# Kernel optimization log

Hardware: AMD Instinct MI355X
Metric: run time of the kernel (lower is better)

## Reference

```python
import jax, jax.numpy as jnp
import numpy as np
from jax import lax

NUM_CLASSES = 16
IMAGE_SHAPE = (512, 512)
CONF_T = 0.05          # confidence_threshold (also NMS score_threshold)
IOU_T = 0.5            # nms_iou_threshold
MAX_PER_CLASS = 100    # max_detections_per_class
MAX_DET = 100          # max_detections
SIGMA = 0.05           # soft_nms_sigma
NEG = -1e10            # finite 'removed' score (always < CONF_T)


def _make_anchors(image_shape=IMAGE_SHAPE):
    # EfficientDet-style anchors: levels 3-7, anchor_scale=4, 3 scales x 3 ratios.
    # Format [cx, cy, w, h] in absolute pixels.
    H, W = image_shape
    out = []
    for level in range(3, 8):
        stride = 2 ** level
        base = float(stride) * 4.0
        fh, fw = H // stride, W // stride
        cx = (np.arange(fw) + 0.5) * stride
        cy = (np.arange(fh) + 0.5) * stride
        cxg, cyg = np.meshgrid(cx, cy)
        centers = np.stack([cxg, cyg], -1).reshape(-1, 1, 2)
        wh = np.array([[base * s * np.sqrt(r), base * s / np.sqrt(r)]
                       for s in (1.0, 2 ** (1.0 / 3.0), 2 ** (2.0 / 3.0))
                       for r in (0.5, 1.0, 2.0)])  # [9,2]
        a = np.concatenate([np.broadcast_to(centers, (fh * fw, 9, 2)),
                            np.broadcast_to(wh[None], (fh * fw, 9, 2))], -1)
        out.append(a.reshape(-1, 4))
    return np.concatenate(out, 0).astype(np.float32)  # [49104, 4]


def setup_inputs() -> dict:
    key = jax.random.key(0)
    N = 49104
    predictions = jax.random.normal(key, (4, N, 4 + NUM_CLASSES), dtype=jnp.float32)
    anchors = jnp.asarray(_make_anchors())
    return {"predictions": predictions, "anchors": anchors}


def _decode_boxes(box_pred, anchors):
    # box_variance is None -> no scaling. anchors [N,4] in [cx,cy,w,h].
    a = anchors[None]                                  # [1,N,4]
    xy = box_pred[..., :2] * a[..., 2:] + a[..., :2]   # centers
    wh = jnp.exp(box_pred[..., 2:]) * a[..., 2:]       # sizes
    return jnp.concatenate([xy - 0.5 * wh, xy + 0.5 * wh], -1)  # corners


def _pairwise_iou(sel, boxes):
    # sel [B,C,4], boxes [B,N,4] -> iou [B,C,N]
    lt = jnp.maximum(sel[:, :, None, :2], boxes[:, None, :, :2])
    rb = jnp.minimum(sel[:, :, None, 2:], boxes[:, None, :, 2:])
    wh = jnp.maximum(rb - lt, 0.0)
    inter = wh[..., 0] * wh[..., 1]
    area_s = (sel[..., 2] - sel[..., 0]) * (sel[..., 3] - sel[..., 1])
    area_b = (boxes[..., 2] - boxes[..., 0]) * (boxes[..., 3] - boxes[..., 1])
    union = area_s[:, :, None] + area_b[:, None, :] - inter
    return jnp.where(union > 0, inter / jnp.where(union > 0, union, 1.0), 0.0)


def _soft_nms(boxes, scores_init, remat=False):
    # Vectorized soft-NMS over all (batch, class) lanes simultaneously.
    # Matches tf.image.non_max_suppression_with_scores (Gaussian soft-NMS):
    # iteratively select max decayed score; hard-suppress iou>thr; decay
    # others by exp(-0.5/sigma * iou^2); stop when max < score_threshold.
    B, C, N = scores_init.shape
    scale = -0.5 / SIGMA
    n_idx = jnp.arange(N)

    def step(scores, _):
        idx = jnp.argmax(scores, axis=-1)                                   # [B,C]
        s = jnp.take_along_axis(scores, idx[..., None], axis=-1)[..., 0]    # [B,C]
        pick = s >= CONF_T
        sel = jax.vmap(lambda bx, ii: bx[ii])(boxes, idx)                   # [B,C,4]
        iou = _pairwise_iou(sel, boxes)                                     # [B,C,N]
        w = jnp.exp(scale * iou * iou)
        new = jnp.where(iou > IOU_T, NEG, scores * w)
        new = jnp.where(n_idx[None, None, :] == idx[..., None], NEG, new)
        scores = jnp.where(pick[..., None], new, scores)
        return scores, (idx, s, pick)

    if remat:
        step = jax.checkpoint(step)
    _, (idxs, sels, picks) = lax.scan(step, scores_init, None, length=MAX_PER_CLASS)
    tr = lambda x: jnp.moveaxis(x, 0, -1)  # [T,B,C] -> [B,C,T]
    return tr(idxs), tr(sels), tr(picks)


def _postprocess(boxes, idxs, sels, picks):
    # Per-class padding to MAX_PER_CLASS, class-major concat, compaction of
    # valid entries, then pad (<= MAX_DET) or stable top-MAX_DET by score.
    B, C, T = picks.shape
    M = C * T
    sel_boxes = jax.vmap(lambda bx, ii: bx[ii])(boxes, idxs.reshape(B, M))  # [B,M,4]
    scores_f = jnp.where(picks, sels, 0.0).reshape(B, M)
    boxes_f = jnp.where(picks.reshape(B, M, 1), sel_boxes, 0.0)
    cls_f = jnp.where(picks, jnp.arange(C, dtype=jnp.int32)[None, :, None],
                      jnp.int32(-1)).reshape(B, M)
    valid = picks.reshape(B, M)
    num_valid = jnp.sum(valid, axis=-1).astype(jnp.int32)                   # [B]

    # stable compaction: valid entries first, original (class-major) order kept
    order = jnp.argsort(jnp.logical_not(valid), axis=-1, stable=True)
    scf = jnp.take_along_axis(scores_f, order, -1)
    bxf = jnp.take_along_axis(boxes_f, order[..., None], 1)
    clf = jnp.take_along_axis(cls_f, order, -1)
    iv = jnp.arange(M)[None] < num_valid[:, None]
    scf = jnp.where(iv, scf, 0.0)
    bxf = jnp.where(iv[..., None], bxf, 0.0)
    clf = jnp.where(iv, clf, jnp.int32(-1))

    # overflow branch: stable descending sort by score over valid entries
    ordB = jnp.argsort(jnp.where(iv, -scf, jnp.inf), axis=-1, stable=True)[:, :MAX_DET]
    over = (num_valid > MAX_DET)[:, None]
    out_sc = jnp.where(over, jnp.take_along_axis(scf, ordB, -1), scf[:, :MAX_DET])
    out_bx = jnp.where(over[..., None],
                       jnp.take_along_axis(bxf, ordB[..., None], 1), bxf[:, :MAX_DET])
    out_cl = jnp.where(over, jnp.take_along_axis(clf, ordB, -1), clf[:, :MAX_DET])
    valid_det = jnp.minimum(num_valid, MAX_DET)
    return valid_det, out_bx, out_sc, out_cl


@jax.jit
def _forward(predictions, anchors):
    boxes = _decode_boxes(predictions[..., :4], anchors)          # [B,N,4]
    cls_prob = jax.nn.sigmoid(predictions[..., 4:])               # [B,N,C]
    max_cls = jnp.argmax(cls_prob, -1)                            # [B,N]
    max_score = jnp.max(cls_prob, -1)
    keep = max_score >= CONF_T
    C = cls_prob.shape[-1]
    cls_mask = (max_cls[:, None, :] == jnp.arange(C)[None, :, None]) & keep[:, None, :]
    scores_init = jnp.where(cls_mask, jnp.swapaxes(cls_prob, 1, 2), NEG)   # [B,C,N]
    idxs, sels, picks = _soft_nms(boxes, scores_init)
    return _postprocess(boxes, idxs, sels, picks)


def reference(predictions, anchors):
    # returns (valid_detections [B], nmsed_boxes [B,100,4],
    #          nmsed_scores [B,100], nmsed_classes [B,100])
    return _forward(predictions, anchors)
```

## Files before the change

kernel.cpp:

```cpp
#include <hip/hip_runtime.h>
#include <math.h>

#define CONF_T 0.05f
#define NEGF  -1e10f
#define NCLS 16
#define TDET 100
#define CAP 4096
#define MSEL 512
#define MTOT (NCLS*TDET)

template<int CTRL>
__device__ __forceinline__ void dpp_comb(float& s, int& j) {
  int si_ = __builtin_amdgcn_update_dpp(__float_as_int(s), __float_as_int(s),
                                        CTRL, 0xf, 0xf, false);
  int ji_ = __builtin_amdgcn_update_dpp(j, j, CTRL, 0xf, 0xf, false);
  float si = __int_as_float(si_);
  bool take = (si > s) || (si == s && ji_ < j);
  s = take ? si : s;
  j = take ? ji_ : j;
}
template<int CTRL>
__device__ __forceinline__ void dpp_max1(float& s) {
  int si_ = __builtin_amdgcn_update_dpp(__float_as_int(s), __float_as_int(s),
                                        CTRL, 0xf, 0xf, false);
  s = fmaxf(s, __int_as_float(si_));
}
template<int CTRL, int RM, bool BC>
__device__ __forceinline__ int dpp_mov0(int v) {
  return __builtin_amdgcn_update_dpp(0, v, CTRL, RM, 0xf, BC);
}
#define ROW_SHR1  0x111
#define ROW_SHR2  0x112
#define ROW_SHR4  0x114
#define ROW_SHR8  0x118
#define ROW_BC15  0x142
#define ROW_BC31  0x143

__device__ __forceinline__ void wave_comb64(float& s, int& j) {
  dpp_comb<ROW_SHR1>(s, j);
  dpp_comb<ROW_SHR2>(s, j);
  dpp_comb<ROW_SHR4>(s, j);
  dpp_comb<ROW_SHR8>(s, j);
  dpp_comb<ROW_BC15>(s, j);
  dpp_comb<ROW_BC31>(s, j);
}
__device__ __forceinline__ void wave_fmax64(float& s) {
  dpp_max1<ROW_SHR1>(s);
  dpp_max1<ROW_SHR2>(s);
  dpp_max1<ROW_SHR4>(s);
  dpp_max1<ROW_SHR8>(s);
  dpp_max1<ROW_BC15>(s);
  dpp_max1<ROW_BC31>(s);
}
__device__ __forceinline__ float rl_f(float v, int l) {
  return __int_as_float(__builtin_amdgcn_readlane(__float_as_int(v), l));
}

__global__ __launch_bounds__(256) void k_decode(
    const float* __restrict__ pred, const float* __restrict__ anch,
    float* __restrict__ boxes, float* __restrict__ score, int* __restrict__ cls,
    int* __restrict__ counts, int N, int nchunk)
{
  #pragma clang fp contract(off)
  const int b = blockIdx.x / nchunk;
  const int chunk = blockIdx.x % nchunk;
  const int t = threadIdx.x;
  const int n = chunk * 256 + t;

  __shared__ int hist[NCLS];
  if (t < NCLS) hist[t] = 0;
  __syncthreads();

  int v = -1;
  if (n < N) {
    const size_t i = (size_t)b * N + n;
    const float4* p4 = reinterpret_cast<const float4*>(pred + i * 20);
    float4 v0 = p4[0], v1 = p4[1], v2 = p4[2], v3 = p4[3], v4 = p4[4];
    float4 a = reinterpret_cast<const float4*>(anch)[n];
    float xx = v0.x * a.z + a.x;
    float yy = v0.y * a.w + a.y;
    float wx = expf(v0.z) * a.z;
    float wy = expf(v0.w) * a.w;
    float hx = 0.5f * wx, hy = 0.5f * wy;
    float4 bx;
    bx.x = xx - hx; bx.y = yy - hy; bx.z = xx + hx; bx.w = yy + hy;
    reinterpret_cast<float4*>(boxes)[i] = bx;

    float lg[NCLS] = {v1.x, v1.y, v1.z, v1.w, v2.x, v2.y, v2.z, v2.w,
                      v3.x, v3.y, v3.z, v3.w, v4.x, v4.y, v4.z, v4.w};
    float best = -1.0f; int bi = 0;
    #pragma unroll
    for (int c = 0; c < NCLS; ++c) {
      float s = 1.0f / (1.0f + expf(-lg[c]));
      if (s > best) { best = s; bi = c; }
    }
    score[i] = best;
    v = (best >= CONF_T) ? bi : -1;
    cls[i] = v;
  }

  int lane = t & 63;
  #pragma unroll
  for (int c = 0; c < NCLS; ++c) {
    unsigned long long bl = __ballot(v == c);
    if (lane == 0 && bl) atomicAdd(&hist[c], __popcll(bl));
  }
  __syncthreads();
  if (t < NCLS) counts[(b * NCLS + t) * nchunk + chunk] = hist[t];
}

__global__ __launch_bounds__(256) void k_scatter(
    const float* __restrict__ score, const int* __restrict__ cls,
    const float* __restrict__ boxes, const int* __restrict__ counts,
    float* __restrict__ cand_sc, float* __restrict__ cand_bx, int* __restrict__ ktot,
    int N, int nchunk)
{
  const int b = blockIdx.x / nchunk;
  const int chunk = blockIdx.x % nchunk;
  const int t = threadIdx.x;
  const int n = chunk * 256 + t;

  __shared__ int s_part[NCLS][17];
  __shared__ int s_ptot[NCLS][17];
  __shared__ int s_off[NCLS];
  __shared__ int wcnt[4][NCLS];

  {
    int c = t >> 4, part = t & 15;
    int su = 0, tot = 0;
    for (int ch = part; ch < nchunk; ch += 16) {
      int vv = counts[(b * NCLS + c) * nchunk + ch];
      tot += vv;
      su += (ch < chunk) ? vv : 0;
    }
    s_part[c][part] = su;
    s_ptot[c][part] = tot;
  }
  __syncthreads();
  if (t < NCLS) {
    int su = 0, tot = 0;
    #pragma unroll
    for (int i = 0; i < 16; ++i) { su += s_part[t][i]; tot += s_ptot[t][i]; }
    s_off[t] = su;
    if (chunk == 0) ktot[b * NCLS + t] = tot;
  }

  int v = (n < N) ? cls[(size_t)b * N + n] : -1;
  int lane = t & 63, w = t >> 6;
  int myrank = 0;
  #pragma unroll
  for (int c = 0; c < NCLS; ++c) {
    unsigned long long bl = __ballot(v == c);
    if (lane == 0) wcnt[w][c] = __popcll(bl);
    if (v == c) myrank = __popcll(bl & ((1ull << lane) - 1ull));
  }
  __syncthreads();
  if (v >= 0) {
    int pre = 0;
    #pragma unroll
    for (int i = 0; i < 4; ++i) if (i < w) pre += wcnt[i][v];
    int pos = s_off[v] + pre + myrank;
    if (pos < CAP) {
      int bc = b * NCLS + v;
      cand_sc[(size_t)bc * CAP + pos] = score[(size_t)b * N + n];
      reinterpret_cast<float4*>(cand_bx)[(size_t)bc * CAP + pos] =
          reinterpret_cast<const float4*>(boxes)[(size_t)b * N + n];
    }
  }
}

__global__ __launch_bounds__(512) void k_nms(
    const float* __restrict__ cand_sc, const float* __restrict__ cand_bx,
    const int* __restrict__ ktot,
    float* __restrict__ out_box, float* __restrict__ out_sc, int* __restrict__ out_pick,
    int* __restrict__ flagOK)
{
  #pragma clang fp contract(off)
  const int bc = blockIdx.x;
  const int t = threadIdx.x;
  const int lane = t & 63, w = t >> 6;

  __shared__ int    hist[4096];
  __shared__ int    s_wsum[8];
  __shared__ int    s_T, s_thrbits;
  __shared__ int    s_cc[8][8];
  __shared__ float  s_csc[MSEL];
  __shared__ float4 sbx[MSEL];
  __shared__ float4 pubA[2][8];
  __shared__ float2 pubB[2][8];
  __shared__ int    s_pk[TDET];
  __shared__ float  s_ps[TDET];

  int K = ktot[bc]; if (K > CAP) K = CAP;

  for (int i = t; i < 4096; i += 512) hist[i] = 0;
  if (t == 0) { s_T = 4096; s_thrbits = 0; }
  __syncthreads();

  float sc[8]; int key[8];
  #pragma unroll
  for (int k = 0; k < 8; ++k) {
    int j = k * 512 + t;
    if (j < K) {
      sc[k] = cand_sc[(size_t)bc * CAP + j];
      int bits = __float_as_int(sc[k]);
      int kk = (bits >> 11) - 0x7E000;
      kk = kk < 0 ? 0 : (kk > 4095 ? 4095 : kk);
      key[k] = kk;
      atomicAdd(&hist[kk], 1);
    } else { key[k] = -1; sc[k] = 0.0f; }
  }
  __syncthreads();

  int h[8]; int loc = 0;
  #pragma unroll
  for (int u = 0; u < 8; ++u) { h[u] = hist[8 * t + u]; loc += h[u]; }
  int pf = loc;
  pf += dpp_mov0<ROW_SHR1, 0xf, true >(pf);
  pf += dpp_mov0<ROW_SHR2, 0xf, true >(pf);
  pf += dpp_mov0<ROW_SHR4, 0xf, true >(pf);
  pf += dpp_mov0<ROW_SHR8, 0xf, true >(pf);
  pf += dpp_mov0<ROW_BC15, 0xa, false>(pf);
  pf += dpp_mov0<ROW_BC31, 0xc, false>(pf);
  if (lane == 63) s_wsum[w] = pf;
  __syncthreads();
  int base = 0, Kall = 0;
  #pragma unroll
  for (int i = 0; i < 8; ++i) {
    int v = s_wsum[i];
    Kall += v;
    if (i < w) base += v;
  }
  {
    int cLE = base + pf;
    int run = Kall - (cLE - loc);
    int cand = 0x7fffffff;
    #pragma unroll
    for (int u = 0; u < 8; ++u) {
      if (cand == 0x7fffffff && run <= MSEL) cand = 8 * t + u;
      run -= h[u];
    }
    if (cand != 0x7fffffff) atomicMin(&s_T, cand);
  }
  __syncthreads();
  const int T = s_T;

  unsigned long long bl0, bl1, bl2, bl3, bl4, bl5, bl6, bl7;
  #define KEEPP(k) ((key[k] >= 0) && (key[k] >= T))
  bl0 = __ballot(KEEPP(0)); bl1 = __ballot(KEEPP(1));
  bl2 = __ballot(KEEPP(2)); bl3 = __ballot(KEEPP(3));
  bl4 = __ballot(KEEPP(4)); bl5 = __ballot(KEEPP(5));
  bl6 = __ballot(KEEPP(6)); bl7 = __ballot(KEEPP(7));
  if (lane == 0) {
    s_cc[w][0] = __popcll(bl0); s_cc[w][1] = __popcll(bl1);
    s_cc[w][2] = __popcll(bl2); s_cc[w][3] = __popcll(bl3);
    s_cc[w][4] = __popcll(bl4); s_cc[w][5] = __popcll(bl5);
    s_cc[w][6] = __popcll(bl6); s_cc[w][7] = __popcll(bl7);
  }
  #pragma unroll
  for (int k = 0; k < 8; ++k)
    if (key[k] >= 0 && key[k] < T) atomicMax(&s_thrbits, __float_as_int(sc[k]));
  __syncthreads();

  int runpos = 0;
  #pragma unroll
  for (int k = 0; k < 8; ++k) {
    int pre = 0, tot = 0;
    #pragma unroll
    for (int i = 0; i < 8; ++i) {
      int c = s_cc[i][k];
      tot += c;
      if (i < w) pre += c;
    }
    unsigned long long blk = (k == 0) ? bl0 : (k == 1) ? bl1 : (k == 2) ? bl2 :
                             (k == 3) ? bl3 : (k == 4) ? bl4 : (k == 5) ? bl5 :
                             (k == 6) ? bl6 : bl7;
    if (KEEPP(k)) {
      int pos = runpos + pre + __popcll(blk & ((1ull << lane) - 1ull));
      s_csc[pos] = sc[k];
      sbx[pos] = reinterpret_cast<const float4*>(cand_bx)[(size_t)bc * CAP + k * 512 + t];
    }
    runpos += tot;
  }
  #undef KEEPP
  const int KM = runpos;
  const float thr = (T == 0) ? -1e30f : __int_as_float(s_thrbits);
  __syncthreads();

  float  rsc0; float4 rbx0; float rar0;
  if (t < KM) {
    rsc0 = s_csc[t];
    rbx0 = sbx[t];
    rar0 = (rbx0.z - rbx0.x) * (rbx0.w - rbx0.y);
  } else {
    rsc0 = NEGF;
    rbx0.x = rbx0.y = rbx0.z = rbx0.w = 0.0f;
    rar0 = 0.0f;
  }

  auto publish = [&](int par) {
    float sm = rsc0;
    wave_fmax64(sm);
    const float smu = rl_f(sm, 63);
    unsigned long long msk = __ballot(rsc0 == smu);
    const int jp = (w << 6) | (int)__builtin_ctzll(msk);
    if (t == jp) {
      float4 ra; ra.x = smu; ra.y = __int_as_float(jp); ra.z = rbx0.x; ra.w = rbx0.y;
      pubA[par][w] = ra;
      float2 r2; r2.x = rbx0.z; r2.y = rbx0.w;
      pubB[par][w] = r2;
    }
  };

  publish(0);

  bool ok = true, early = false;
  int total = 0;
  for (int iter = 0; iter < TDET; ++iter) {
    __syncthreads();
    const int par = iter & 1;

    float4 ra = pubA[par][lane & 7];
    float2 r2 = pubB[par][lane & 7];
    float m = ra.x;
    dpp_max1<ROW_SHR1>(m);
    dpp_max1<ROW_SHR2>(m);
    dpp_max1<ROW_SHR4>(m);
    const float ms = rl_f(m, 7);
    if (ms < CONF_T) { early = true; break; }
    ok = ok && (ms > thr);

    const int r = (int)__builtin_ctzll(__ballot(ra.x == ms));
    const int mj = __builtin_amdgcn_readlane(__float_as_int(ra.y), r);
    const float px = rl_f(ra.z, r);
    const float py = rl_f(ra.w, r);
    const float pz = rl_f(r2.x, r);
    const float pw = rl_f(r2.y, r);
    if (t == 0) { s_pk[iter] = mj; s_ps[iter] = ms; }
    total = iter + 1;
    const float pa = (pz - px) * (pw - py);

    if (rsc0 != NEGF) {
      if (t == mj) {
        rsc0 = NEGF;
      } else if (!(px > rbx0.z || pz < rbx0.x || py > rbx0.w || pw < rbx0.y)) {
        float ltx = fmaxf(px, rbx0.x);
        float lty = fmaxf(py, rbx0.y);
        float rbv = fminf(pz, rbx0.z);
        float rby = fminf(pw, rbx0.w);
        float wx = fmaxf(rbv - ltx, 0.0f);
        float wy = fmaxf(rby - lty, 0.0f);
        float inter = wx * wy;
        if (inter > 0.0f) {
          float iou = inter / ((pa + rar0) - inter);
          float ns;
          if (iou > 0.5f) ns = NEGF;
          else {
            ns = rsc0 * expf((-10.0f * iou) * iou);
            if (ns < CONF_T) ns = NEGF;
          }
          rsc0 = ns;
        }
      }
    }

    publish(par ^ 1);
  }
  if (early) ok = ok && (thr < CONF_T);

  __syncthreads();
  float* ob  = out_box  + (size_t)bc * TDET * 4;
  float* osc = out_sc   + (size_t)bc * TDET;
  int*   opk = out_pick + (size_t)bc * TDET;
  for (int rr = total + t; rr < TDET; rr += 512) opk[rr] = 0;
  if (t < total) {
    int jp = s_pk[t];
    float4 pb = sbx[jp];
    ob[t * 4 + 0] = pb.x; ob[t * 4 + 1] = pb.y;
    ob[t * 4 + 2] = pb.z; ob[t * 4 + 3] = pb.w;
    osc[t] = s_ps[t];
    opk[t] = 1;
  }
  if (t == 0) flagOK[bc] = ok ? 1 : 0;
}

__global__ __launch_bounds__(1024) void k_nms_full(
    const float* __restrict__ cand_sc, const float* __restrict__ cand_bx,
    const int* __restrict__ ktot, const int* __restrict__ flagOK,
    float* __restrict__ out_box, float* __restrict__ out_sc, int* __restrict__ out_pick)
{
  #pragma clang fp contract(off)
  const int bc = blockIdx.x;
  if (flagOK[bc]) return;
  const int t = threadIdx.x;
  const int lane = t & 63, w = t >> 6;

  __shared__ float4 s_box[CAP];
  __shared__ float  pub_s[64];
  __shared__ int    pub_j[64];
  __shared__ int    s_pkj[TDET];
  __shared__ float  s_pks[TDET];
  __shared__ int    s_info[2];

  int K = ktot[bc]; if (K > CAP) K = CAP;

  float  rsc[4];
  float4 rbx[4];
  float  rar[4];
  #pragma unroll
  for (int k = 0; k < 4; ++k) {
    int j = k * 1024 + t;
    if (j < K) {
      rsc[k] = cand_sc[(size_t)bc * CAP + j];
      float4 bb = reinterpret_cast<const float4*>(cand_bx)[(size_t)bc * CAP + j];
      rbx[k] = bb;
      s_box[j] = bb;
      rar[k] = (bb.z - bb.x) * (bb.w - bb.y);
    } else {
      rsc[k] = NEGF;
      rbx[k].x = rbx[k].y = rbx[k].z = rbx[k].w = 0.0f;
      float4 z; z.x = z.y = z.z = z.w = 0.0f;
      s_box[j] = z;
      rar[k] = 0.0f;
    }
  }

  auto publish4 = [&]() {
    float a0 = rsc[0], a1 = rsc[1], a2 = rsc[2], a3 = rsc[3];
    #pragma unroll
    for (int r = 0; r < 4; ++r) {
      float bs = a0; int bk = 0;
      if (a1 > bs) { bs = a1; bk = 1; }
      if (a2 > bs) { bs = a2; bk = 2; }
      if (a3 > bs) { bs = a3; bk = 3; }
      float s1 = bs; int j1 = bk * 1024 + t;
      wave_comb64(s1, j1);
      int ju = __builtin_amdgcn_readlane(j1, 63);
      if ((ju & 1023) == t) {
        int ex = ju >> 10;
        if (ex == 0) a0 = NEGF; else if (ex == 1) a1 = NEGF;
        else if (ex == 2) a2 = NEGF; else a3 = NEGF;
      }
      if (lane == 63) { pub_s[w * 4 + r] = s1; pub_j[w * 4 + r] = j1; }
    }
  };

  publish4();

  int total = 0;
  while (true) {
    __syncthreads();
    if (w == 0) {
      float es = pub_s[lane];
      int   ej = pub_j[lane];
      float4 eb = s_box[ej];
      float ear = (eb.z - eb.x) * (eb.w - eb.y);
      bool  eav = (es >= CONF_T);
      float hv = ((lane & 3) == 3) ? es : NEGF;
      wave_fmax64(hv);
      const float H = rl_f(hv, 63);
      int Rr = 0, dn = 0;
      while (true) {
        float cs = eav ? es : NEGF;
        int   cj = eav ? ej : 0x7fffffff;
        wave_comb64(cs, cj);
        float ms = rl_f(cs, 63);
        int   mj = __builtin_amdgcn_readlane(cj, 63);
        if (ms < CONF_T) { if (H < CONF_T) dn = 1; break; }
        if (Rr > 0 && !(ms > H)) break;
        if (lane == 0) { s_pkj[total + Rr] = mj; s_pks[total + Rr] = ms; }
        Rr++;
        if (total + Rr >= TDET) { dn = 1; break; }
        float4 pb = s_box[mj];
        float pa = (pb.z - pb.x) * (pb.w - pb.y);
        if (eav) {
          if (ej == mj) { eav = false; }
          else {
            float ltx = fmaxf(pb.x, eb.x);
            float lty = fmaxf(pb.y, eb.y);
            float rbv = fminf(pb.z, eb.z);
            float rby = fminf(pb.w, eb.w);
            float wx = fmaxf(rbv - ltx, 0.0f);
            float wy = fmaxf(rby - lty, 0.0f);
            float inter = wx * wy;
            if (inter > 0.0f) {
              float iou = inter / ((pa + ear) - inter);
              if (iou > 0.5f) { eav = false; }
              else {
                es = es * expf((-10.0f * iou) * iou);
                if (es < CONF_T) eav = false;
              }
            }
          }
        }
      }
      if (lane == 0) { s_info[0] = Rr; s_info[1] = dn; }
    }
    __syncthreads();

    const int Rr = s_info[0];
    const int dn = s_info[1];
    for (int r = 0; r < Rr; ++r) {
      const int jp = s_pkj[total + r];
      float4 pb = s_box[jp];
      float pa = (pb.z - pb.x) * (pb.w - pb.y);
      #pragma unroll
      for (int k = 0; k < 4; ++k) {
        float s = rsc[k];
        if (s == NEGF) continue;
        if (k * 1024 + t == jp) { rsc[k] = NEGF; continue; }
        float ltx = fmaxf(pb.x, rbx[k].x);
        float lty = fmaxf(pb.y, rbx[k].y);
        float rbv = fminf(pb.z, rbx[k].z);
        float rby = fminf(pb.w, rbx[k].w);
        float wx = fmaxf(rbv - ltx, 0.0f);
        float wy = fmaxf(rby - lty, 0.0f);
        float inter = wx * wy;
        if (inter > 0.0f) {
          float iou = inter / ((pa + rar[k]) - inter);
          float ns;
          if (iou > 0.5f) ns = NEGF;
          else {
            ns = s * expf((-10.0f * iou) * iou);
            if (ns < CONF_T) ns = NEGF;
          }
          rsc[k] = ns;
        }
      }
    }
    total += Rr;
    if (dn) break;
    publish4();
  }

  float* ob  = out_box  + (size_t)bc * TDET * 4;
  float* osc = out_sc   + (size_t)bc * TDET;
  int*   opk = out_pick + (size_t)bc * TDET;
  if (t < TDET) {
    if (t < total) {
      int jp = s_pkj[t];
      float4 pb = s_box[jp];
      ob[t * 4 + 0] = pb.x; ob[t * 4 + 1] = pb.y;
      ob[t * 4 + 2] = pb.z; ob[t * 4 + 3] = pb.w;
      osc[t] = s_pks[t];
      opk[t] = 1;
    } else {
      opk[t] = 0;
    }
  }
}

__global__ __launch_bounds__(1024) void k_post(
    const float* __restrict__ out_box, const float* __restrict__ out_sc,
    const int* __restrict__ out_pick,
    float* __restrict__ out, int B)
{
  #pragma clang fp contract(off)
  const int b = blockIdx.x;
  const int t = threadIdx.x;

  __shared__ float p_sc[MTOT];
  __shared__ float p_bx[MTOT * 4];
  __shared__ unsigned char p_v[MTOT];
  __shared__ float q_sc[MTOT];
  __shared__ short q_m[MTOT];
  __shared__ int s_wtot[16];
  __shared__ unsigned long long s_key[2048];

  for (int m = t; m < MTOT; m += 1024) {
    int c = m / TDET, tt = m % TDET;
    int lanebc = b * NCLS + c;
    int pk = out_pick[(size_t)lanebc * TDET + tt];
    p_v[m] = (unsigned char)pk;
    if (pk) {
      p_sc[m] = out_sc[(size_t)lanebc * TDET + tt];
      p_bx[m * 4 + 0] = out_box[((size_t)lanebc * TDET + tt) * 4 + 0];
      p_bx[m * 4 + 1] = out_box[((size_t)lanebc * TDET + tt) * 4 + 1];
      p_bx[m * 4 + 2] = out_box[((size_t)lanebc * TDET + tt) * 4 + 2];
      p_bx[m * 4 + 3] = out_box[((size_t)lanebc * TDET + tt) * 4 + 3];
    } else {
      p_sc[m] = 0.0f;
      p_bx[m * 4 + 0] = 0.0f; p_bx[m * 4 + 1] = 0.0f;
      p_bx[m * 4 + 2] = 0.0f; p_bx[m * 4 + 3] = 0.0f;
    }
  }
  __syncthreads();

  int running = 0;
  for (int base = 0; base < MTOT; base += 1024) {
    int m = base + t;
    bool v = (m < MTOT) && p_v[m];
    unsigned long long ball = __ballot(v);
    int lane = t & 63, w = t >> 6;
    if (lane == 0) s_wtot[w] = __popcll(ball);
    __syncthreads();
    int off = 0, tot = 0;
    #pragma unroll
    for (int i = 0; i < 16; ++i) {
      int ci = s_wtot[i];
      if (i < w) off += ci;
      tot += ci;
    }
    if (v) {
      int wpre = __popcll(ball & ((1ull << lane) - 1ull));
      int j = running + off + wpre;
      q_sc[j] = p_sc[m];
      q_m[j] = (short)m;
    }
    running += tot;
    __syncthreads();
  }
  int nv = running;
  bool over = nv > TDET;

  if (over) {
    for (int e = t; e < 2048; e += 1024) {
      unsigned long long kk = 0;
      if (e < nv) {
        unsigned int sb = __float_as_uint(q_sc[e]);
        kk = ((unsigned long long)sb << 32) | (unsigned int)(~e);
      }
      s_key[e] = ~kk;
    }
    for (int kk2 = 2; kk2 <= 2048; kk2 <<= 1) {
      for (int j = kk2 >> 1; j > 0; j >>= 1) {
        __syncthreads();
        int e = ((t & ~(j - 1)) << 1) | (t & (j - 1));
        int q = e | j;
        unsigned long long a = s_key[e], bb = s_key[q];
        bool up = ((e & kk2) == 0);
        bool sw = up ? (a > bb) : (a < bb);
        if (sw) { s_key[e] = bb; s_key[q] = a; }
      }
    }
    __syncthreads();
  }

  int vd = nv < TDET ? nv : TDET;
  int base_box = B;
  int base_sc  = B + B * TDET * 4;
  int base_cl  = base_sc + B * TDET;
  if (t == 0) out[b] = (float)vd;
  if (t < TDET) {
    float sc = 0.0f, cl = -1.0f, b0 = 0.0f, b1 = 0.0f, b2 = 0.0f, b3 = 0.0f;
    int p = -1;
    if (t < nv) p = over ? (int)(unsigned int)s_key[t] : t;
    if (p >= 0) {
      int m = q_m[p];
      sc = q_sc[p];
      cl = (float)(m / TDET);
      b0 = p_bx[m * 4 + 0]; b1 = p_bx[m * 4 + 1];
      b2 = p_bx[m * 4 + 2]; b3 = p_bx[m * 4 + 3];
    }
    int o = b * TDET + t;
    out[base_box + o * 4 + 0] = b0;
    out[base_box + o * 4 + 1] = b1;
    out[base_box + o * 4 + 2] = b2;
    out[base_box + o * 4 + 3] = b3;
    out[base_sc + o] = sc;
    out[base_cl + o] = cl;
  }
}

extern "C" void kernel_launch(void* const* d_in, const int* in_sizes, int n_in,
                              void* d_out, int out_size, void* d_ws, size_t ws_size,
                              hipStream_t stream) {
  const float* pred = (const float*)d_in[0];
  const float* anch = (const float*)d_in[1];
  int N  = in_sizes[1] / 4;
  int BN = in_sizes[0] / 20;
  int B  = BN / N;
  int nchunk = (N + 255) / 256;
  int NBC = B * NCLS;

  char* ws = (char*)d_ws;
  size_t off = 0;
  float* boxes  = (float*)(ws + off); off += (size_t)BN * 4 * sizeof(float);
  float* candbx = (float*)(ws + off); off += (size_t)NBC * CAP * 4 * sizeof(float);
  float* obox   = (float*)(ws + off); off += (size_t)NBC * TDET * 4 * sizeof(float);
  float* score  = (float*)(ws + off); off += (size_t)BN * sizeof(float);
  float* candsc = (float*)(ws + off); off += (size_t)NBC * CAP * sizeof(float);
  float* osc    = (float*)(ws + off); off += (size_t)NBC * TDET * sizeof(float);
  int*   cls    = (int*)(ws + off);   off += (size_t)BN * sizeof(int);
  int*   counts = (int*)(ws + off);   off += (size_t)NBC * nchunk * sizeof(int);
  int*   ktot   = (int*)(ws + off);   off += (size_t)NBC * sizeof(int);
  int*   opick  = (int*)(ws + off);   off += (size_t)NBC * TDET * sizeof(int);
  int*   flagOK = (int*)(ws + off);   off += (size_t)NBC * sizeof(int);

  k_decode<<<B * nchunk, 256, 0, stream>>>(pred, anch, boxes, score, cls, counts, N, nchunk);
  k_scatter<<<B * nchunk, 256, 0, stream>>>(score, cls, boxes, counts, candsc, candbx, ktot, N, nchunk);
  k_nms<<<NBC, 512, 0, stream>>>(candsc, candbx, ktot, obox, osc, opick, flagOK);
  k_nms_full<<<NBC, 1024, 0, stream>>>(candsc, candbx, ktot, flagOK, obox, osc, opick);
  k_post<<<B, 1024, 0, stream>>>(obox, osc, opick, (float*)d_out, B);
}
```

Baseline: 123.7 us.

## Move box decode into scatter and cache per-wave max in soft-NMS loop

```diff
diff --git a/kernel.cpp b/kernel.cpp
--- a/kernel.cpp
+++ b/kernel.cpp
@@ -57,8 +57,8 @@
 }
 
 __global__ __launch_bounds__(256) void k_decode(
-    const float* __restrict__ pred, const float* __restrict__ anch,
-    float* __restrict__ boxes, float* __restrict__ score, int* __restrict__ cls,
+    const float* __restrict__ pred,
+    float* __restrict__ score, int* __restrict__ cls,
     int* __restrict__ counts, int N, int nchunk)
 {
   #pragma clang fp contract(off)
@@ -75,17 +75,7 @@
   if (n < N) {
     const size_t i = (size_t)b * N + n;
     const float4* p4 = reinterpret_cast<const float4*>(pred + i * 20);
-    float4 v0 = p4[0], v1 = p4[1], v2 = p4[2], v3 = p4[3], v4 = p4[4];
-    float4 a = reinterpret_cast<const float4*>(anch)[n];
-    float xx = v0.x * a.z + a.x;
-    float yy = v0.y * a.w + a.y;
-    float wx = expf(v0.z) * a.z;
-    float wy = expf(v0.w) * a.w;
-    float hx = 0.5f * wx, hy = 0.5f * wy;
-    float4 bx;
-    bx.x = xx - hx; bx.y = yy - hy; bx.z = xx + hx; bx.w = yy + hy;
-    reinterpret_cast<float4*>(boxes)[i] = bx;
-
+    float4 v1 = p4[1], v2 = p4[2], v3 = p4[3], v4 = p4[4];
     float lg[NCLS] = {v1.x, v1.y, v1.z, v1.w, v2.x, v2.y, v2.z, v2.w,
                       v3.x, v3.y, v3.z, v3.w, v4.x, v4.y, v4.z, v4.w};
     float best = -1.0f; int bi = 0;
@@ -110,11 +100,13 @@
 }
 
 __global__ __launch_bounds__(256) void k_scatter(
+    const float* __restrict__ pred, const float* __restrict__ anch,
     const float* __restrict__ score, const int* __restrict__ cls,
-    const float* __restrict__ boxes, const int* __restrict__ counts,
+    const int* __restrict__ counts,
     float* __restrict__ cand_sc, float* __restrict__ cand_bx, int* __restrict__ ktot,
     int N, int nchunk)
 {
+  #pragma clang fp contract(off)
   const int b = blockIdx.x / nchunk;
   const int chunk = blockIdx.x % nchunk;
   const int t = threadIdx.x;
@@ -161,10 +153,19 @@
     for (int i = 0; i < 4; ++i) if (i < w) pre += wcnt[i][v];
     int pos = s_off[v] + pre + myrank;
     if (pos < CAP) {
+      const size_t i = (size_t)b * N + n;
+      float4 p0 = *reinterpret_cast<const float4*>(pred + i * 20);
+      float4 a = reinterpret_cast<const float4*>(anch)[n];
+      float xx = p0.x * a.z + a.x;
+      float yy = p0.y * a.w + a.y;
+      float wx = expf(p0.z) * a.z;
+      float wy = expf(p0.w) * a.w;
+      float hx = 0.5f * wx, hy = 0.5f * wy;
+      float4 bx;
+      bx.x = xx - hx; bx.y = yy - hy; bx.z = xx + hx; bx.w = yy + hy;
       int bc = b * NCLS + v;
-      cand_sc[(size_t)bc * CAP + pos] = score[(size_t)b * N + n];
-      reinterpret_cast<float4*>(cand_bx)[(size_t)bc * CAP + pos] =
-          reinterpret_cast<const float4*>(boxes)[(size_t)b * N + n];
+      cand_sc[(size_t)bc * CAP + pos] = score[i];
+      reinterpret_cast<float4*>(cand_bx)[(size_t)bc * CAP + pos] = bx;
     }
   }
 }
@@ -186,8 +187,7 @@
   __shared__ int    s_cc[8][8];
   __shared__ float  s_csc[MSEL];
   __shared__ float4 sbx[MSEL];
-  __shared__ float4 pubA[2][8];
-  __shared__ float2 pubB[2][8];
+  __shared__ float4 pub[2][16];
   __shared__ int    s_pk[TDET];
   __shared__ float  s_ps[TDET];
 
@@ -298,21 +298,29 @@
     rar0 = 0.0f;
   }
 
-  auto publish = [&](int par) {
-    float sm = rsc0;
-    wave_fmax64(sm);
-    const float smu = rl_f(sm, 63);
-    unsigned long long msk = __ballot(rsc0 == smu);
-    const int jp = (w << 6) | (int)__builtin_ctzll(msk);
-    if (t == jp) {
-      float4 ra; ra.x = smu; ra.y = __int_as_float(jp); ra.z = rbx0.x; ra.w = rbx0.y;
-      pubA[par][w] = ra;
-      float2 r2; r2.x = rbx0.z; r2.y = rbx0.w;
-      pubB[par][w] = r2;
+  float ps = NEGF, p1 = 0.0f, p2 = 0.0f, p3 = 0.0f, p4v = 0.0f;
+  int   pj = 0;
+
+  auto publish = [&](int par, bool recompute) {
+    if (recompute) {
+      float sm = rsc0;
+      wave_fmax64(sm);
+      ps = rl_f(sm, 63);
+      unsigned long long msk = __ballot(rsc0 == ps);
+      int jl = (int)__builtin_ctzll(msk);
+      pj = (w << 6) | jl;
+      p1 = rl_f(rbx0.x, jl); p2 = rl_f(rbx0.y, jl);
+      p3 = rl_f(rbx0.z, jl); p4v = rl_f(rbx0.w, jl);
+    }
+    if (lane == 0) {
+      float4 ra; ra.x = ps; ra.y = __int_as_float(pj); ra.z = p1; ra.w = p2;
+      pub[par][w] = ra;
+      float4 rb; rb.x = p3; rb.y = p4v; rb.z = 0.0f; rb.w = 0.0f;
+      pub[par][8 + w] = rb;
     }
   };
 
-  publish(0);
+  publish(0, true);
 
   bool ok = true, early = false;
   int total = 0;
@@ -320,29 +328,30 @@
     __syncthreads();
     const int par = iter & 1;
 
-    float4 ra = pubA[par][lane & 7];
-    float2 r2 = pubB[par][lane & 7];
-    float m = ra.x;
+    float4 ra = pub[par][lane & 15];
+    float m = ((lane & 15) < 8) ? ra.x : NEGF;
     dpp_max1<ROW_SHR1>(m);
     dpp_max1<ROW_SHR2>(m);
     dpp_max1<ROW_SHR4>(m);
-    const float ms = rl_f(m, 7);
+    const float ms = rl_f(m, 0);
     if (ms < CONF_T) { early = true; break; }
     ok = ok && (ms > thr);
 
-    const int r = (int)__builtin_ctzll(__ballot(ra.x == ms));
+    const int r = (int)__builtin_ctzll(
+        __ballot(((lane & 15) < 8) && (ra.x == ms)));
     const int mj = __builtin_amdgcn_readlane(__float_as_int(ra.y), r);
     const float px = rl_f(ra.z, r);
     const float py = rl_f(ra.w, r);
-    const float pz = rl_f(r2.x, r);
-    const float pw = rl_f(r2.y, r);
+    const float pz = rl_f(ra.x, 8 + r);
+    const float pw = rl_f(ra.y, 8 + r);
     if (t == 0) { s_pk[iter] = mj; s_ps[iter] = ms; }
     total = iter + 1;
     const float pa = (pz - px) * (pw - py);
 
+    bool chg = false;
     if (rsc0 != NEGF) {
       if (t == mj) {
-        rsc0 = NEGF;
+        rsc0 = NEGF; chg = true;
       } else if (!(px > rbx0.z || pz < rbx0.x || py > rbx0.w || pw < rbx0.y)) {
         float ltx = fmaxf(px, rbx0.x);
         float lty = fmaxf(py, rbx0.y);
@@ -359,12 +368,12 @@
             ns = rsc0 * expf((-10.0f * iou) * iou);
             if (ns < CONF_T) ns = NEGF;
           }
-          rsc0 = ns;
+          rsc0 = ns; chg = true;
         }
       }
     }
 
-    publish(par ^ 1);
+    publish(par ^ 1, __ballot(chg) != 0ull);
   }
   if (early) ok = ok && (thr < CONF_T);
 
@@ -675,7 +684,6 @@
 
   char* ws = (char*)d_ws;
   size_t off = 0;
-  float* boxes  = (float*)(ws + off); off += (size_t)BN * 4 * sizeof(float);
   float* candbx = (float*)(ws + off); off += (size_t)NBC * CAP * 4 * sizeof(float);
   float* obox   = (float*)(ws + off); off += (size_t)NBC * TDET * 4 * sizeof(float);
   float* score  = (float*)(ws + off); off += (size_t)BN * sizeof(float);
@@ -687,8 +695,9 @@
   int*   opick  = (int*)(ws + off);   off += (size_t)NBC * TDET * sizeof(int);
   int*   flagOK = (int*)(ws + off);   off += (size_t)NBC * sizeof(int);
 
-  k_decode<<<B * nchunk, 256, 0, stream>>>(pred, anch, boxes, score, cls, counts, N, nchunk);
-  k_scatter<<<B * nchunk, 256, 0, stream>>>(score, cls, boxes, counts, candsc, candbx, ktot, N, nchunk);
+  k_decode<<<B * nchunk, 256, 0, stream>>>(pred, score, cls, counts, N, nchunk);
+  k_scatter<<<B * nchunk, 256, 0, stream>>>(pred, anch, score, cls, counts,
+                                            candsc, candbx, ktot, N, nchunk);
   k_nms<<<NBC, 512, 0, stream>>>(candsc, candbx, ktot, obox, osc, opick, flagOK);
   k_nms_full<<<NBC, 1024, 0, stream>>>(candsc, candbx, ktot, flagOK, obox, osc, opick);
   k_post<<<B, 1024, 0, stream>>>(obox, osc, opick, (float*)d_out, B);
```

After: 275.8 us. +123.0%, slower.
